# Kernel optimization log

Measured on AMD Instinct MI355X. Metric: run time of the kernel, lower is better.

Reference implementation:

```python
import jax, jax.numpy as jnp
import numpy as np

N, D, C_CLS = 8192, 512, 1000
SCALE = 1.0
LOW_THRE = 1.0 / C_CLS
EPS = 1e-12  # torch F.normalize eps


def _l2norm(x):
    n = jnp.sqrt(jnp.sum(x * x, axis=1, keepdims=True))
    return x / jnp.maximum(n, EPS)


def setup_inputs() -> dict:
    key = jax.random.key(0)
    k1, k2, k3, k4, k5 = jax.random.split(key, 5)
    feature = jax.random.normal(k1, (N, D), jnp.float32)
    proxy_raw = jax.random.normal(k2, (C_CLS, D), jnp.float32) * 0.02
    cP_weight = jax.random.normal(k3, (D, D), jnp.float32) * 0.05
    # probability-like rows (sum to 1), as prob_detach is a detached softmax output
    prob_detach = jax.nn.softmax(4.0 * jax.random.normal(k4, (N, C_CLS), jnp.float32), axis=-1)
    conf_mask = jax.random.randint(k5, (N,), 0, 2) > 0
    return {"feature": feature, "proxy_raw": proxy_raw, "cP_weight": cP_weight,
            "prob_detach": prob_detach, "conf_mask": conf_mask}


def reference(feature, proxy_raw, cP_weight, prob_detach, conf_mask):
    feat = _l2norm(feature)                                   # (N, D)
    proxy = _l2norm(proxy_raw @ cP_weight.T)                  # (C, D), cP is a linear projection

    class_candidates = prob_detach > LOW_THRE                 # (N, C) bool
    top1_idx = jnp.argmax(prob_detach, axis=1)                # (N,)
    top1_class = jnp.arange(C_CLS)[None, :] == top1_idx[:, None]  # (N, C) bool one-hot

    not_conf = ~conf_mask
    pred_class = (class_candidates & not_conf[:, None]) | (top1_class & conf_mask[:, None])  # (N, C)

    # sc_proxy: (sc_weight.unsqueeze(2) * proxy).sum(dim=1) == matmul
    sc_weight = prob_detach * class_candidates                # (N, C)
    sc_proxy = sc_weight @ proxy                              # (N, D)
    sc_sim = jnp.sum(feat * sc_proxy, axis=1)                 # (N,)

    pred = feat @ proxy.T                                     # (N, C)
    proxy_sim = jnp.take_along_axis(pred, top1_idx[:, None], axis=1)[:, 0]  # (N,)
    pos_pair = jnp.where(conf_mask, proxy_sim, sc_sim)        # (N,)

    # intersection.any(dim=2) == (pred_class @ pred_class.T) > 0 (avoids (N,N,C) tensor)
    pc = pred_class.astype(feat.dtype)
    neg_matrix = ~((pc @ pc.T) > 0)                           # (N, N) bool

    sim = feat @ feat.T                                       # (N, N)
    sim = sim * neg_matrix
    neg_pair = jnp.where(sim < 1e-6, -jnp.inf, sim)           # masked_fill

    logits = jnp.concatenate([pos_pair[:, None], neg_pair], axis=1)  # (N, N+1)
    logp = jax.nn.log_softmax(SCALE * logits, axis=1)
    loss = -jnp.mean(logp[:, 0])                              # nll_loss with label 0

    denom = jnp.sum(not_conf)
    sc_count = jnp.sum(class_candidates & not_conf[:, None])
    sc_num = jnp.where(denom > 0,
                       sc_count.astype(jnp.float32) / jnp.maximum(denom, 1).astype(jnp.float32),
                       jnp.float32(0.0))
    return loss, sc_num
```

## Files before the change

### kernel.cpp

```cpp
#include <hip/hip_runtime.h>
#include <hip/hip_bf16.h>

#define N_ROWS 8192
#define DIM 512
#define C_CLSN 1000
#define C_PAD 1024
#define LOW_THRE (1.0f / 1000.0f)
#define LDK 40
#define LDF8 72

typedef __bf16 bf16x8 __attribute__((ext_vector_type(8)));
typedef float floatx4 __attribute__((ext_vector_type(4)));
typedef unsigned long long ull;
typedef ull ull2 __attribute__((ext_vector_type(2)));


__global__ __launch_bounds__(1024) void kzp_v12(const int* __restrict__ conf,
                                                int* __restrict__ perm,
                                                int* __restrict__ counters) {
  int tid = threadIdx.x;
  __shared__ int sc[1024];
  __shared__ int sbad, sodd1, seven1, smode;
  if (tid == 0) { sbad = 0; sodd1 = 0; seven1 = 0; }
  __syncthreads();
  for (int i = tid; i < 2048; i += 1024) {
    int v = conf[i];
    if (v != 0 && v != 1) atomicOr(&sbad, 1);
    if (v == 1) { if (i & 1) atomicAdd(&sodd1, 1); else atomicAdd(&seven1, 1); }
  }
  __syncthreads();
  if (tid == 0) {
    int mode = 0;
    if (sbad) mode = 1;
    else if (seven1 > 0 && sodd1 == 0) mode = 2;
    smode = mode;
  }
  __syncthreads();
  int mode = smode;
  int r0 = tid * 8;
  int f[8]; int cnt = 0;
  #pragma unroll
  for (int k = 0; k < 8; ++k) {
    int r = r0 + k;
    bool c;
    if (mode == 1)      c = ((const unsigned char*)conf)[r] != 0;
    else if (mode == 2) c = ((const long long*)conf)[r] != 0;
    else                c = conf[r] != 0;
    f[k] = c ? 1 : 0; cnt += f[k];
  }
  sc[tid] = cnt;
  __syncthreads();
  for (int off = 1; off < 1024; off <<= 1) {
    int v = (tid >= off) ? sc[tid - off] : 0;
    __syncthreads();
    sc[tid] += v;
    __syncthreads();
  }
  int incl = sc[tid];
  int excl = incl - cnt;
  int total = sc[1023];
  if (tid == 0) counters[3] = total;
  int cpos = excl;
  int npos = total + (r0 - excl);
  #pragma unroll
  for (int k = 0; k < 8; ++k) {
    if (f[k]) perm[cpos++] = r0 + k;
    else      perm[npos++] = r0 + k;
  }
}

__global__ __launch_bounds__(256) void kda_v12(const float* __restrict__ prob,
                                               const float* __restrict__ feature,
                                               const int* __restrict__ perm,
                                               const int* __restrict__ counters_ro,
                                               ull* __restrict__ bits,
                                               int* __restrict__ top1a,
                                               int* __restrict__ cnta,
                                               __bf16* __restrict__ featBF,
                                               unsigned char* __restrict__ featF8) {
  int wv = threadIdx.x >> 6, lane = threadIdx.x & 63;
  int p = blockIdx.x * 4 + wv;
  int orig = perm[p];
  bool is_conf = p < counters_ro[3];
  const float4* pr4 = (const float4*)(prob + (size_t)orig * C_CLSN);
  float4 v[4];
  #pragma unroll
  for (int pass = 0; pass < 4; ++pass) {
    int q = pass * 64 + lane;
    v[pass] = (q < 250) ? pr4[q] : make_float4(-1.f, -1.f, -1.f, -1.f);
  }
  float bv = -1e30f; int bidx = 0x7fffffff;
  int cnt = 0;
  ull myword = 0ULL;
  #pragma unroll
  for (int pass = 0; pass < 4; ++pass) {
    int q = pass * 64 + lane;
    bool inb = q < 250;
    float el[4] = {v[pass].x, v[pass].y, v[pass].z, v[pass].w};
    #pragma unroll
    for (int j = 0; j < 4; ++j) {
      float pv = el[j];
      int c = q * 4 + j;
      if (inb && pv > bv) { bv = pv; bidx = c; }
      ull m = __ballot(inb && (pv > LOW_THRE));
      cnt += (int)__popcll(m);
      if (lane == pass * 4 + j) myword = m;
    }
  }
  #pragma unroll
  for (int m = 1; m < 64; m <<= 1) {
    float ov = __shfl_xor(bv, m); int oi = __shfl_xor(bidx, m);
    if (ov > bv || (ov == bv && oi < bidx)) { bv = ov; bidx = oi; }
  }
  int top1 = bidx;
  if (is_conf) {
    int w1 = ((top1 >> 8) << 2) | (top1 & 3);
    myword = (lane == w1) ? (1ULL << ((top1 >> 2) & 63)) : 0ULL;
  }
  if (lane < 16) bits[(size_t)p * 16 + lane] = myword;
  if (lane == 0) {
    top1a[p] = top1;
    cnta[p] = is_conf ? 0 : cnt;
  }
  const float* fr = feature + (size_t)orig * DIM;
  int c0 = lane * 8;
  float4 v0 = *(const float4*)(fr + c0);
  float4 v1 = *(const float4*)(fr + c0 + 4);
  float ss = v0.x*v0.x + v0.y*v0.y + v0.z*v0.z + v0.w*v0.w
           + v1.x*v1.x + v1.y*v1.y + v1.z*v1.z + v1.w*v1.w;
  #pragma unroll
  for (int m = 1; m < 64; m <<= 1) ss += __shfl_xor(ss, m);
  float scl = 1.0f / fmaxf(sqrtf(ss), 1e-12f);
  float x0 = v0.x*scl, x1 = v0.y*scl, x2 = v0.z*scl, x3 = v0.w*scl;
  float x4 = v1.x*scl, x5 = v1.y*scl, x6 = v1.z*scl, x7 = v1.w*scl;
  bf16x8 bvx;
  bvx[0] = (__bf16)x0; bvx[1] = (__bf16)x1; bvx[2] = (__bf16)x2; bvx[3] = (__bf16)x3;
  bvx[4] = (__bf16)x4; bvx[5] = (__bf16)x5; bvx[6] = (__bf16)x6; bvx[7] = (__bf16)x7;
  *(bf16x8*)(featBF + (size_t)p * DIM + c0) = bvx;
  int lo = __builtin_amdgcn_cvt_pk_fp8_f32(x0, x1, 0, false);
  lo = __builtin_amdgcn_cvt_pk_fp8_f32(x2, x3, lo, true);
  int hi = __builtin_amdgcn_cvt_pk_fp8_f32(x4, x5, 0, false);
  hi = __builtin_amdgcn_cvt_pk_fp8_f32(x6, x7, hi, true);
  int2 pk; pk.x = lo; pk.y = hi;
  *(int2*)(featF8 + (size_t)p * DIM + c0) = pk;
}

__global__ __launch_bounds__(256) void kbc_v12(const float* __restrict__ raw,
                                               const float* __restrict__ cP,
                                               __bf16* __restrict__ proxyBF) {
  int tid = threadIdx.x;
  int c0 = blockIdx.x * 8;
  int d0 = tid, d1 = tid + 256;
  if (c0 >= C_CLSN) {
    #pragma unroll
    for (int cc = 0; cc < 8; ++cc) {
      proxyBF[(size_t)(c0 + cc) * DIM + d0] = (__bf16)0.f;
      proxyBF[(size_t)(c0 + cc) * DIM + d1] = (__bf16)0.f;
    }
    return;
  }
  __shared__ float sraw[8 * DIM];
  __shared__ float red[8 * 256];
  for (int idx = tid; idx < 8 * DIM; idx += 256)
    sraw[idx] = raw[(size_t)c0 * DIM + idx];
  __syncthreads();
  float acc0[8], acc1[8];
  #pragma unroll
  for (int cc = 0; cc < 8; ++cc) { acc0[cc] = 0.f; acc1[cc] = 0.f; }
  for (int k = 0; k < DIM; k += 4) {
    float4 w0 = *(const float4*)&cP[(size_t)d0 * DIM + k];
    float4 w1 = *(const float4*)&cP[(size_t)d1 * DIM + k];
    #pragma unroll
    for (int cc = 0; cc < 8; ++cc) {
      const float* sr = &sraw[cc * DIM + k];
      acc0[cc] += sr[0]*w0.x + sr[1]*w0.y + sr[2]*w0.z + sr[3]*w0.w;
      acc1[cc] += sr[0]*w1.x + sr[1]*w1.y + sr[2]*w1.z + sr[3]*w1.w;
    }
  }
  #pragma unroll
  for (int cc = 0; cc < 8; ++cc)
    red[cc * 256 + tid] = acc0[cc]*acc0[cc] + acc1[cc]*acc1[cc];
  __syncthreads();
  for (int s = 128; s > 0; s >>= 1) {
    if (tid < s)
      #pragma unroll
      for (int cc = 0; cc < 8; ++cc)
        red[cc * 256 + tid] += red[cc * 256 + tid + s];
    __syncthreads();
  }
  #pragma unroll
  for (int cc = 0; cc < 8; ++cc) {
    float scl = 1.0f / fmaxf(sqrtf(red[cc * 256]), 1e-12f);
    proxyBF[(size_t)(c0 + cc) * DIM + d0] = (__bf16)(acc0[cc] * scl);
    proxyBF[(size_t)(c0 + cc) * DIM + d1] = (__bf16)(acc1[cc] * scl);
  }
}

__global__ __launch_bounds__(512) void kegg_v12(const __bf16* __restrict__ featBF,
                                                const __bf16* __restrict__ proxyBF,
                                                const unsigned char* __restrict__ featF8,
                                                const float* __restrict__ prob,
                                                const ull* __restrict__ bits,
                                                const int* __restrict__ perm,
                                                const int* __restrict__ top1a,
                                                const int* __restrict__ counters_ro,
                                                float* __restrict__ scsim,
                                                float* __restrict__ possim,
                                                float* __restrict__ S) {
  __shared__ __align__(16) char smem[35840];
  int tid = threadIdx.x;
  int wv = tid >> 6, lane = tid & 63;
  int wi = wv >> 2, wj = wv & 3;
  int lr = lane >> 4, lc = lane & 15;

  floatx4 acc[4][2];
  floatx4 zero = {0.f, 0.f, 0.f, 0.f};
  #pragma unroll
  for (int ti = 0; ti < 4; ++ti)
    #pragma unroll
    for (int tj = 0; tj < 2; ++tj) acc[ti][tj] = zero;

  if (blockIdx.x < 512) {
    __bf16* As = (__bf16*)smem;
    __bf16* Bs = (__bf16*)(smem + 10240);
    int* pO  = (int*)(smem + 20480);
    int* t1r = (int*)(smem + 20992);
    int bi = blockIdx.x >> 3;
    int bj = blockIdx.x & 7;
    if (tid < 128) { pO[tid] = perm[bi * 128 + tid]; t1r[tid] = top1a[bi * 128 + tid]; }
    const __bf16* Abase = featBF + (size_t)bi * 128 * DIM;
    const __bf16* Bbase = proxyBF + (size_t)bj * 128 * DIM;
    for (int kt = 0; kt < DIM; kt += 32) {
      __syncthreads();
      {
        int rw = tid >> 2, cc = (tid & 3) * 8;
        *(bf16x8*)&As[rw * LDK + cc] = *(const bf16x8*)&Abase[(size_t)rw * DIM + kt + cc];
        *(bf16x8*)&Bs[rw * LDK + cc] = *(const bf16x8*)&Bbase[(size_t)rw * DIM + kt + cc];
      }
      __syncthreads();
      bf16x8 afr[4], bfr[2];
      #pragma unroll
      for (int ti = 0; ti < 4; ++ti)
        afr[ti] = *(bf16x8*)&As[(wi * 64 + ti * 16 + lc) * LDK + lr * 8];
      #pragma unroll
      for (int tj = 0; tj < 2; ++tj)
        bfr[tj] = *(bf16x8*)&Bs[(wj * 32 + tj * 16 + lc) * LDK + lr * 8];
      #pragma unroll
      for (int ti = 0; ti < 4; ++ti)
        #pragma unroll
        for (int tj = 0; tj < 2; ++tj)
          acc[ti][tj] = __builtin_amdgcn_mfma_f32_16x16x32_bf16(afr[ti], bfr[tj], acc[ti][tj], 0, 0, 0);
    }
    __syncthreads();
    #pragma unroll
    for (int ti = 0; ti < 4; ++ti) {
      int ibase = wi * 64 + ti * 16 + lr * 4;
      float rs[4] = {0.f, 0.f, 0.f, 0.f};
      #pragma unroll
      for (int rr = 0; rr < 4; ++rr) {
        int il = ibase + rr;
        int orig = pO[il];
        int t1 = t1r[il];
        const float* prow = prob + (size_t)orig * C_CLSN;
        #pragma unroll
        for (int tj = 0; tj < 2; ++tj) {
          int c = bj * 128 + wj * 32 + tj * 16 + lc;
          float P = acc[ti][tj][rr];
          float pv = (c < C_CLSN) ? prow[c] : 0.f;
          if (pv > LOW_THRE) rs[rr] += pv * P;
          if (c == t1) possim[bi * 128 + il] = P;
        }
      }
      #pragma unroll
      for (int m = 1; m < 16; m <<= 1)
        #pragma unroll
        for (int rr = 0; rr < 4; ++rr) rs[rr] += __shfl_xor(rs[rr], m);
      if (lc == 0) {
        #pragma unroll
        for (int rr = 0; rr < 4; ++rr)
          atomicAdd(&scsim[bi * 128 + ibase + rr], rs[rr]);
      }
    }
    return;
  }

  unsigned char* As = (unsigned char*)smem;
  unsigned char* Bs = (unsigned char*)(smem + 9216);
  ull* bsJ = (ull*)smem;
  ull* bsI = (ull*)(smem + 18432);
  int* t1I = (int*)(smem + 34816);
  int* t1J = (int*)(smem + 35328);

  int b = (int)(((long long)(blockIdx.x - 512) * 997) % 2080);
  int bi = 0, rem = b;
  while (rem >= 64 - bi) { rem -= 64 - bi; bi++; }
  int bj = bi + rem;

  int nconf = counters_ro[3];
  bool allcI = (bi * 128 + 128) <= nconf;
  bool allcJ = (bj * 128 + 128) <= nconf;
  int mode = allcJ ? 0 : (allcI ? 1 : 3);

  if (tid < 128)      t1I[tid]       = top1a[bi * 128 + tid];
  else if (tid < 256) t1J[tid - 128] = top1a[bj * 128 + tid - 128];
  if (mode == 3) {
    #pragma unroll
    for (int e = 0; e < 4; ++e) {
      int flat = tid + e * 512;
      int row = flat & 127, w = flat >> 7;
      bsI[w * 128 + row] = bits[(size_t)(bi * 128 + row) * 16 + w];
    }
  }

  int rw = tid >> 2, cc = (tid & 3) * 16;
  const unsigned char* Aptr = featF8 + (size_t)(bi * 128 + rw) * DIM + cc;
  const unsigned char* Bptr = featF8 + (size_t)(bj * 128 + rw) * DIM + cc;
  int4 pa = *(const int4*)Aptr;
  int4 pb = *(const int4*)Bptr;

  for (int kt = 0; kt < DIM; kt += 64) {
    __syncthreads();
    *(int4*)&As[rw * LDF8 + cc] = pa;
    *(int4*)&Bs[rw * LDF8 + cc] = pb;
    __syncthreads();
    if (kt + 64 < DIM) {
      pa = *(const int4*)(Aptr + kt + 64);
      pb = *(const int4*)(Bptr + kt + 64);
    }
    #pragma unroll
    for (int ks = 0; ks < 2; ++ks) {
      long a_[4], b_[2];
      #pragma unroll
      for (int ti = 0; ti < 4; ++ti)
        a_[ti] = *(const long*)&As[(wi * 64 + ti * 16 + lc) * LDF8 + ks * 32 + lr * 8];
      #pragma unroll
      for (int tj = 0; tj < 2; ++tj)
        b_[tj] = *(const long*)&Bs[(wj * 32 + tj * 16 + lc) * LDF8 + ks * 32 + lr * 8];
      #pragma unroll
      for (int ti = 0; ti < 4; ++ti)
        #pragma unroll
        for (int tj = 0; tj < 2; ++tj)
          acc[ti][tj] = __builtin_amdgcn_mfma_f32_16x16x32_fp8_fp8(a_[ti], b_[tj], acc[ti][tj], 0, 0, 0);
    }
  }
  __syncthreads();
  if (mode != 0) {
    #pragma unroll
    for (int e = 0; e < 4; ++e) {
      int flat = tid + e * 512;
      int row = flat & 127, w = flat >> 7;
      bsJ[w * 128 + row] = bits[(size_t)(bj * 128 + row) * 16 + w];
    }
  }
  __syncthreads();

  int tJv[2];
  #pragma unroll
  for (int tj = 0; tj < 2; ++tj) tJv[tj] = t1J[wj * 32 + tj * 16 + lc];

  float cs[2] = {0.f, 0.f};
  #pragma unroll
  for (int ti = 0; ti < 4; ++ti) {
    int ibase = wi * 64 + ti * 16 + lr * 4;
    unsigned inter[8];
    if (mode == 0) {
      #pragma unroll
      for (int rr = 0; rr < 4; ++rr) {
        int tI = t1I[ibase + rr];
        #pragma unroll
        for (int tj = 0; tj < 2; ++tj) inter[rr * 2 + tj] = (tI == tJv[tj]);
      }
    } else if (mode == 1) {
      #pragma unroll
      for (int rr = 0; rr < 4; ++rr) {
        int tI = t1I[ibase + rr];
        int w = ((tI >> 8) << 2) | (tI & 3);
        int bb = (tI >> 2) & 63;
        #pragma unroll
        for (int tj = 0; tj < 2; ++tj) {
          ull word = bsJ[w * 128 + wj * 32 + tj * 16 + lc];
          inter[rr * 2 + tj] = (unsigned)((word >> bb) & 1ULL);
        }
      }
    } else {
      #pragma unroll
      for (int q = 0; q < 8; ++q) inter[q] = 0u;
      #pragma unroll
      for (int w = 0; w < 16; ++w) {
        ull2 a01 = *(const ull2*)&bsI[w * 128 + ibase];
        ull2 a23 = *(const ull2*)&bsI[w * 128 + ibase + 2];
        ull aw[4] = {a01[0], a01[1], a23[0], a23[1]};
        ull bw[2];
        #pragma unroll
        for (int tj = 0; tj < 2; ++tj) bw[tj] = bsJ[w * 128 + wj * 32 + tj * 16 + lc];
        #pragma unroll
        for (int rr = 0; rr < 4; ++rr)
          #pragma unroll
          for (int tj = 0; tj < 2; ++tj) {
            ull t = aw[rr] & bw[tj];
            inter[rr * 2 + tj] |= (unsigned)(t | (t >> 32));
          }
      }
    }
    float rs[4] = {0.f, 0.f, 0.f, 0.f};
    #pragma unroll
    for (int rr = 0; rr < 4; ++rr)
      #pragma unroll
      for (int tj = 0; tj < 2; ++tj) {
        float sim = acc[ti][tj][rr];
        sim = fminf(sim, 1.0f);
        float e_ = ((inter[rr * 2 + tj] == 0u) && (sim >= 1e-6f)) ? __expf(sim) : 0.f;
        rs[rr] += e_;
        cs[tj] += e_;
      }
    #pragma unroll
    for (int m = 1; m < 16; m <<= 1)
      #pragma unroll
      for (int rr = 0; rr < 4; ++rr) rs[rr] += __shfl_xor(rs[rr], m);
    if (lc == 0) {
      #pragma unroll
      for (int rr = 0; rr < 4; ++rr)
        atomicAdd(&S[(size_t)bi * 128 + ibase + rr], rs[rr]);
    }
  }
  if (bi != bj) {
    #pragma unroll
    for (int tj = 0; tj < 2; ++tj) {
      cs[tj] += __shfl_xor(cs[tj], 16);
      cs[tj] += __shfl_xor(cs[tj], 32);
    }
    if (lr == 0) {
      #pragma unroll
      for (int tj = 0; tj < 2; ++tj)
        atomicAdd(&S[(size_t)bj * 128 + wj * 32 + tj * 16 + lc], cs[tj]);
    }
  }
}

__global__ __launch_bounds__(1024) void kf_final_v12(const float* __restrict__ possim,
                                                     const float* __restrict__ scsim,
                                                     const float* __restrict__ S,
                                                     const int* __restrict__ cnta,
                                                     const int* __restrict__ counters,
                                                     float* __restrict__ out) {
  __shared__ float red[1024];
  __shared__ int redi[1024];
  int tid = threadIdx.x;
  int nconf = counters[3];
  float local = 0.f;
  int lcnt = 0;
  for (int i = tid; i < N_ROWS; i += 1024) {
    float p = (i < nconf) ? possim[i] : scsim[i];
    p = fminf(fmaxf(p, -1.1f), 1.1f);
    float s = fmaxf(S[i], 0.0f);
    local += logf(expf(p) + s) - p;
    lcnt += cnta[i];
  }
  red[tid] = local;
  redi[tid] = lcnt;
  __syncthreads();
  for (int s = 512; s > 0; s >>= 1) {
    if (tid < s) { red[tid] += red[tid + s]; redi[tid] += redi[tid + s]; }
    __syncthreads();
  }
  if (tid == 0) {
    float loss = red[0] / (float)N_ROWS;
    int denom = N_ROWS - nconf;
    int scc = redi[0];
    float scn = (denom > 0) ? ((float)scc / (float)denom) : 0.f;
    out[0] = loss;
    out[1] = scn;
  }
}

extern "C" void kernel_launch(void* const* d_in, const int* in_sizes, int n_in,
                              void* d_out, int out_size, void* d_ws, size_t ws_size,
                              hipStream_t stream) {
  const float* feature   = (const float*)d_in[0];
  const float* proxy_raw = (const float*)d_in[1];
  const float* cP        = (const float*)d_in[2];
  const float* prob      = (const float*)d_in[3];
  const int*   conf      = (const int*)d_in[4];
  float* out = (float*)d_out;

  size_t need = (size_t)N_ROWS * DIM * 2
              + (size_t)N_ROWS * DIM
              + (size_t)C_PAD * DIM * 2
              + (size_t)N_ROWS * 16 * 8
              + (size_t)N_ROWS * 4
              + (size_t)N_ROWS * 4
              + (size_t)N_ROWS * 4
              + 256
              + (size_t)N_ROWS * 4
              + (size_t)N_ROWS * 4
              + (size_t)N_ROWS * 4;
  if (ws_size < need) return;

  char* ws = (char*)d_ws;
  __bf16* featBF  = (__bf16*)ws;              ws += (size_t)N_ROWS * DIM * 2;
  unsigned char* featF8 = (unsigned char*)ws; ws += (size_t)N_ROWS * DIM;
  __bf16* proxyBF = (__bf16*)ws;              ws += (size_t)C_PAD * DIM * 2;
  ull* bits       = (ull*)ws;                 ws += (size_t)N_ROWS * 16 * 8;
  float* possim   = (float*)ws;               ws += (size_t)N_ROWS * 4;
  float* S        = (float*)ws;               ws += (size_t)N_ROWS * 4;
  float* scsim    = (float*)ws;               ws += (size_t)N_ROWS * 4;
  int* counters   = (int*)ws;                 ws += 256;
  int* perm       = (int*)ws;                 ws += (size_t)N_ROWS * 4;
  int* top1a      = (int*)ws;                 ws += (size_t)N_ROWS * 4;
  int* cnta       = (int*)ws;                 ws += (size_t)N_ROWS * 4;

  hipMemsetAsync(S, 0, (size_t)N_ROWS * 8 + 256, stream);
  kzp_v12<<<1, 1024, 0, stream>>>(conf, perm, counters);
  kda_v12<<<N_ROWS / 4, 256, 0, stream>>>(prob, feature, perm, counters,
                                          bits, top1a, cnta, featBF, featF8);
  kbc_v12<<<C_PAD / 8, 256, 0, stream>>>(proxy_raw, cP, proxyBF);
  kegg_v12<<<512 + 2080, 512, 0, stream>>>(featBF, proxyBF, featF8, prob, bits, perm,
                                           top1a, counters, scsim, possim, S);
  kf_final_v12<<<1, 1024, 0, stream>>>(possim, scsim, S, cnta, counters, out);
}
```

Before: 312.8 us.

## Store features and proxies in MFMA fragment layout and load operands directly

The normalization kernels now write bf16/fp8 features and bf16 proxies in a blocked layout of 16-row groups that matches the MFMA operand fragment order. Each lane can then load its fragments straight from global memory with contiguous accesses. This drops the LDS staging tiles and the per-k-step barriers in both the proxy GEMM and the N×N similarity GEMM, and an occupancy hint of 4 blocks is added. The cost is that operands are re-read from global/L2 by every wave instead of being shared through LDS, and the K loop no longer prefetches the next tile.

```diff
diff --git a/kernel.cpp b/kernel.cpp
--- a/kernel.cpp
+++ b/kernel.cpp
@@ -6,8 +6,6 @@
 #define C_CLSN 1000
 #define C_PAD 1024
 #define LOW_THRE (1.0f / 1000.0f)
-#define LDK 40
-#define LDF8 72
 
 typedef __bf16 bf16x8 __attribute__((ext_vector_type(8)));
 typedef float floatx4 __attribute__((ext_vector_type(4)));
@@ -15,7 +13,8 @@
 typedef ull ull2 __attribute__((ext_vector_type(2)));
 
 
-__global__ __launch_bounds__(1024) void kzp_v12(const int* __restrict__ conf,
+
+__global__ __launch_bounds__(1024) void kzp_v13(const int* __restrict__ conf,
                                                 int* __restrict__ perm,
                                                 int* __restrict__ counters) {
   int tid = threadIdx.x;
@@ -69,7 +68,7 @@
   }
 }
 
-__global__ __launch_bounds__(256) void kda_v12(const float* __restrict__ prob,
+__global__ __launch_bounds__(256) void kda_v13(const float* __restrict__ prob,
                                                const float* __restrict__ feature,
                                                const int* __restrict__ perm,
                                                const int* __restrict__ counters_ro,
@@ -136,26 +135,31 @@
   bf16x8 bvx;
   bvx[0] = (__bf16)x0; bvx[1] = (__bf16)x1; bvx[2] = (__bf16)x2; bvx[3] = (__bf16)x3;
   bvx[4] = (__bf16)x4; bvx[5] = (__bf16)x5; bvx[6] = (__bf16)x6; bvx[7] = (__bf16)x7;
-  *(bf16x8*)(featBF + (size_t)p * DIM + c0) = bvx;
+  int g = p >> 4, r = p & 15;
+  *(bf16x8*)((char*)featBF + (size_t)g * 16384 + (size_t)lane * 256 + (size_t)r * 16) = bvx;
   int lo = __builtin_amdgcn_cvt_pk_fp8_f32(x0, x1, 0, false);
   lo = __builtin_amdgcn_cvt_pk_fp8_f32(x2, x3, lo, true);
   int hi = __builtin_amdgcn_cvt_pk_fp8_f32(x4, x5, 0, false);
   hi = __builtin_amdgcn_cvt_pk_fp8_f32(x6, x7, hi, true);
   int2 pk; pk.x = lo; pk.y = hi;
-  *(int2*)(featF8 + (size_t)p * DIM + c0) = pk;
+  *(int2*)(featF8 + (size_t)g * 8192 + (size_t)lane * 128 + (size_t)r * 8) = pk;
 }
 
-__global__ __launch_bounds__(256) void kbc_v12(const float* __restrict__ raw,
+__global__ __launch_bounds__(256) void kbc_v13(const float* __restrict__ raw,
                                                const float* __restrict__ cP,
                                                __bf16* __restrict__ proxyBF) {
   int tid = threadIdx.x;
   int c0 = blockIdx.x * 8;
   int d0 = tid, d1 = tid + 256;
+  int g = c0 >> 4;
+  int r0 = c0 & 15;
+  char* pbase = (char*)proxyBF + (size_t)g * 16384;
   if (c0 >= C_CLSN) {
     #pragma unroll
     for (int cc = 0; cc < 8; ++cc) {
-      proxyBF[(size_t)(c0 + cc) * DIM + d0] = (__bf16)0.f;
-      proxyBF[(size_t)(c0 + cc) * DIM + d1] = (__bf16)0.f;
+      int row = r0 + cc;
+      *(__bf16*)(pbase + (size_t)(d0 >> 3) * 256 + row * 16 + (d0 & 7) * 2) = (__bf16)0.f;
+      *(__bf16*)(pbase + (size_t)(d1 >> 3) * 256 + row * 16 + (d1 & 7) * 2) = (__bf16)0.f;
     }
     return;
   }
@@ -191,23 +195,24 @@
   #pragma unroll
   for (int cc = 0; cc < 8; ++cc) {
     float scl = 1.0f / fmaxf(sqrtf(red[cc * 256]), 1e-12f);
-    proxyBF[(size_t)(c0 + cc) * DIM + d0] = (__bf16)(acc0[cc] * scl);
-    proxyBF[(size_t)(c0 + cc) * DIM + d1] = (__bf16)(acc1[cc] * scl);
+    int row = r0 + cc;
+    *(__bf16*)(pbase + (size_t)(d0 >> 3) * 256 + row * 16 + (d0 & 7) * 2) = (__bf16)(acc0[cc] * scl);
+    *(__bf16*)(pbase + (size_t)(d1 >> 3) * 256 + row * 16 + (d1 & 7) * 2) = (__bf16)(acc1[cc] * scl);
   }
 }
 
-__global__ __launch_bounds__(512) void kegg_v12(const __bf16* __restrict__ featBF,
-                                                const __bf16* __restrict__ proxyBF,
-                                                const unsigned char* __restrict__ featF8,
-                                                const float* __restrict__ prob,
-                                                const ull* __restrict__ bits,
-                                                const int* __restrict__ perm,
-                                                const int* __restrict__ top1a,
-                                                const int* __restrict__ counters_ro,
-                                                float* __restrict__ scsim,
-                                                float* __restrict__ possim,
-                                                float* __restrict__ S) {
-  __shared__ __align__(16) char smem[35840];
+__global__ __launch_bounds__(512, 4) void kegg_v13(const __bf16* __restrict__ featBF,
+                                                   const __bf16* __restrict__ proxyBF,
+                                                   const unsigned char* __restrict__ featF8,
+                                                   const float* __restrict__ prob,
+                                                   const ull* __restrict__ bits,
+                                                   const int* __restrict__ perm,
+                                                   const int* __restrict__ top1a,
+                                                   const int* __restrict__ counters_ro,
+                                                   float* __restrict__ scsim,
+                                                   float* __restrict__ possim,
+                                                   float* __restrict__ S) {
+  __shared__ __align__(16) char smem[33792];
   int tid = threadIdx.x;
   int wv = tid >> 6, lane = tid & 63;
   int wi = wv >> 2, wj = wv & 3;
@@ -221,37 +226,35 @@
     for (int tj = 0; tj < 2; ++tj) acc[ti][tj] = zero;
 
   if (blockIdx.x < 512) {
-    __bf16* As = (__bf16*)smem;
-    __bf16* Bs = (__bf16*)(smem + 10240);
-    int* pO  = (int*)(smem + 20480);
-    int* t1r = (int*)(smem + 20992);
+    int* pO  = (int*)smem;
+    int* t1r = (int*)(smem + 512);
     int bi = blockIdx.x >> 3;
     int bj = blockIdx.x & 7;
     if (tid < 128) { pO[tid] = perm[bi * 128 + tid]; t1r[tid] = top1a[bi * 128 + tid]; }
-    const __bf16* Abase = featBF + (size_t)bi * 128 * DIM;
-    const __bf16* Bbase = proxyBF + (size_t)bj * 128 * DIM;
+    __syncthreads();
+    const char* A = (const char*)featBF;
+    const char* B = (const char*)proxyBF;
+    size_t aO[4], bO[2];
+    #pragma unroll
+    for (int ti = 0; ti < 4; ++ti)
+      aO[ti] = (size_t)(bi * 8 + wi * 4 + ti) * 16384 + (size_t)lane * 16;
+    #pragma unroll
+    for (int tj = 0; tj < 2; ++tj)
+      bO[tj] = (size_t)(bj * 8 + wj * 2 + tj) * 16384 + (size_t)lane * 16;
     for (int kt = 0; kt < DIM; kt += 32) {
-      __syncthreads();
-      {
-        int rw = tid >> 2, cc = (tid & 3) * 8;
-        *(bf16x8*)&As[rw * LDK + cc] = *(const bf16x8*)&Abase[(size_t)rw * DIM + kt + cc];
-        *(bf16x8*)&Bs[rw * LDK + cc] = *(const bf16x8*)&Bbase[(size_t)rw * DIM + kt + cc];
-      }
-      __syncthreads();
       bf16x8 afr[4], bfr[2];
       #pragma unroll
       for (int ti = 0; ti < 4; ++ti)
-        afr[ti] = *(bf16x8*)&As[(wi * 64 + ti * 16 + lc) * LDK + lr * 8];
+        afr[ti] = *(const bf16x8*)(A + aO[ti] + (size_t)kt * 32);
       #pragma unroll
       for (int tj = 0; tj < 2; ++tj)
-        bfr[tj] = *(bf16x8*)&Bs[(wj * 32 + tj * 16 + lc) * LDK + lr * 8];
+        bfr[tj] = *(const bf16x8*)(B + bO[tj] + (size_t)kt * 32);
       #pragma unroll
       for (int ti = 0; ti < 4; ++ti)
         #pragma unroll
         for (int tj = 0; tj < 2; ++tj)
           acc[ti][tj] = __builtin_amdgcn_mfma_f32_16x16x32_bf16(afr[ti], bfr[tj], acc[ti][tj], 0, 0, 0);
     }
-    __syncthreads();
     #pragma unroll
     for (int ti = 0; ti < 4; ++ti) {
       int ibase = wi * 64 + ti * 16 + lr * 4;
@@ -284,12 +287,10 @@
     return;
   }
 
-  unsigned char* As = (unsigned char*)smem;
-  unsigned char* Bs = (unsigned char*)(smem + 9216);
-  ull* bsJ = (ull*)smem;
-  ull* bsI = (ull*)(smem + 18432);
-  int* t1I = (int*)(smem + 34816);
-  int* t1J = (int*)(smem + 35328);
+  ull* bsI = (ull*)smem;
+  ull* bsJ = (ull*)(smem + 16384);
+  int* t1I = (int*)(smem + 32768);
+  int* t1J = (int*)(smem + 33280);
 
   int b = (int)(((long long)(blockIdx.x - 512) * 997) % 2080);
   int bi = 0, rem = b;
@@ -311,39 +312,6 @@
       bsI[w * 128 + row] = bits[(size_t)(bi * 128 + row) * 16 + w];
     }
   }
-
-  int rw = tid >> 2, cc = (tid & 3) * 16;
-  const unsigned char* Aptr = featF8 + (size_t)(bi * 128 + rw) * DIM + cc;
-  const unsigned char* Bptr = featF8 + (size_t)(bj * 128 + rw) * DIM + cc;
-  int4 pa = *(const int4*)Aptr;
-  int4 pb = *(const int4*)Bptr;
-
-  for (int kt = 0; kt < DIM; kt += 64) {
-    __syncthreads();
-    *(int4*)&As[rw * LDF8 + cc] = pa;
-    *(int4*)&Bs[rw * LDF8 + cc] = pb;
-    __syncthreads();
-    if (kt + 64 < DIM) {
-      pa = *(const int4*)(Aptr + kt + 64);
-      pb = *(const int4*)(Bptr + kt + 64);
-    }
-    #pragma unroll
-    for (int ks = 0; ks < 2; ++ks) {
-      long a_[4], b_[2];
-      #pragma unroll
-      for (int ti = 0; ti < 4; ++ti)
-        a_[ti] = *(const long*)&As[(wi * 64 + ti * 16 + lc) * LDF8 + ks * 32 + lr * 8];
-      #pragma unroll
-      for (int tj = 0; tj < 2; ++tj)
-        b_[tj] = *(const long*)&Bs[(wj * 32 + tj * 16 + lc) * LDF8 + ks * 32 + lr * 8];
-      #pragma unroll
-      for (int ti = 0; ti < 4; ++ti)
-        #pragma unroll
-        for (int tj = 0; tj < 2; ++tj)
-          acc[ti][tj] = __builtin_amdgcn_mfma_f32_16x16x32_fp8_fp8(a_[ti], b_[tj], acc[ti][tj], 0, 0, 0);
-    }
-  }
-  __syncthreads();
   if (mode != 0) {
     #pragma unroll
     for (int e = 0; e < 4; ++e) {
@@ -353,6 +321,34 @@
     }
   }
   __syncthreads();
+
+  const char* F = (const char*)featF8;
+  size_t aO[4], bO[2];
+  #pragma unroll
+  for (int ti = 0; ti < 4; ++ti)
+    aO[ti] = (size_t)(bi * 8 + wi * 4 + ti) * 8192 + (size_t)lane * 8;
+  #pragma unroll
+  for (int tj = 0; tj < 2; ++tj)
+    bO[tj] = (size_t)(bj * 8 + wj * 2 + tj) * 8192 + (size_t)lane * 8;
+
+  #pragma unroll
+  for (int kt = 0; kt < DIM; kt += 64) {
+    #pragma unroll
+    for (int ks = 0; ks < 2; ++ks) {
+      long a_[4], b_[2];
+      #pragma unroll
+      for (int ti = 0; ti < 4; ++ti)
+        a_[ti] = *(const long*)(F + aO[ti] + (size_t)(kt * 16 + ks * 512));
+      #pragma unroll
+      for (int tj = 0; tj < 2; ++tj)
+        b_[tj] = *(const long*)(F + bO[tj] + (size_t)(kt * 16 + ks * 512));
+      #pragma unroll
+      for (int ti = 0; ti < 4; ++ti)
+        #pragma unroll
+        for (int tj = 0; tj < 2; ++tj)
+          acc[ti][tj] = __builtin_amdgcn_mfma_f32_16x16x32_fp8_fp8(a_[ti], b_[tj], acc[ti][tj], 0, 0, 0);
+    }
+  }
 
   int tJv[2];
   #pragma unroll
@@ -437,7 +433,7 @@
   }
 }
 
-__global__ __launch_bounds__(1024) void kf_final_v12(const float* __restrict__ possim,
+__global__ __launch_bounds__(1024) void kf_final_v13(const float* __restrict__ possim,
                                                      const float* __restrict__ scsim,
                                                      const float* __restrict__ S,
                                                      const int* __restrict__ cnta,
@@ -510,11 +506,11 @@
   int* cnta       = (int*)ws;                 ws += (size_t)N_ROWS * 4;
 
   hipMemsetAsync(S, 0, (size_t)N_ROWS * 8 + 256, stream);
-  kzp_v12<<<1, 1024, 0, stream>>>(conf, perm, counters);
-  kda_v12<<<N_ROWS / 4, 256, 0, stream>>>(prob, feature, perm, counters,
+  kzp_v13<<<1, 1024, 0, stream>>>(conf, perm, counters);
+  kda_v13<<<N_ROWS / 4, 256, 0, stream>>>(prob, feature, perm, counters,
                                           bits, top1a, cnta, featBF, featF8);
-  kbc_v12<<<C_PAD / 8, 256, 0, stream>>>(proxy_raw, cP, proxyBF);
-  kegg_v12<<<512 + 2080, 512, 0, stream>>>(featBF, proxyBF, featF8, prob, bits, perm,
+  kbc_v13<<<C_PAD / 8, 256, 0, stream>>>(proxy_raw, cP, proxyBF);
+  kegg_v13<<<512 + 2080, 512, 0, stream>>>(featBF, proxyBF, featF8, prob, bits, perm,
                                            top1a, counters, scsim, possim, S);
-  kf_final_v12<<<1, 1024, 0, stream>>>(possim, scsim, S, cnta, counters, out);
+  kf_final_v13<<<1, 1024, 0, stream>>>(possim, scsim, S, cnta, counters, out);
 }
```

Result: slower. 359.2 us (+14.8%).
